# Performance work log

Hardware: AMD Instinct MI355X
Metric: run time of the kernel (lower is better)

## Reference

```python
import jax, jax.numpy as jnp
import numpy as np
import math

B, N, D, H = 4, 2048, 256, 4
DH = D // H
EPS = 1e-8


def setup_inputs() -> dict:
    key = jax.random.key(0)
    ks = jax.random.split(key, 8)
    x = jax.random.normal(ks[0], (B, N, D), dtype=jnp.float32)
    # RoPE rotation freqs: exp(i * pos * inv_freq), stored as (cos, sin) pairs -> [N, DH//2, 2]
    d2 = DH // 2
    inv_freq = 1.0 / (10000.0 ** (jnp.arange(d2, dtype=jnp.float32) / d2))
    ang = jnp.arange(N, dtype=jnp.float32)[:, None] * inv_freq[None, :]
    freqs = jnp.stack([jnp.cos(ang), jnp.sin(ang)], axis=-1)  # [N, d2, 2]
    s = 0.02
    g = jnp.ones((D,), dtype=jnp.float32)
    w_qkv = jax.random.normal(ks[1], (D, 3 * D), dtype=jnp.float32) * s
    b_qkv = jnp.zeros((3 * D,), dtype=jnp.float32)
    w_out = jax.random.normal(ks[2], (D, D), dtype=jnp.float32) * s
    b_out = jnp.zeros((D,), dtype=jnp.float32)
    w_gate = jax.random.normal(ks[3], (D, D), dtype=jnp.float32) * s
    b_gate = jnp.zeros((D,), dtype=jnp.float32)
    return {"x": x, "freqs": freqs, "g": g, "w_qkv": w_qkv, "b_qkv": b_qkv,
            "w_out": w_out, "b_out": b_out, "w_gate": w_gate, "b_gate": b_gate}


def _zcrmsnorm(x, g):
    x0 = x - jnp.mean(x, axis=-1, keepdims=True)
    rms = jnp.sqrt(jnp.mean(x0 * x0, axis=-1, keepdims=True) + EPS)
    return x0 / rms * g


def _rope(q, freqs):
    # q: [B,H,N,DH]; freqs: [N,DH//2,2] (cos,sin). Complex multiply on adjacent pairs.
    b, h, n, dh = q.shape
    qp = q.reshape(b, h, n, dh // 2, 2)
    cos = freqs[:n, :, 0][None, None]  # [1,1,N,d2]
    sin = freqs[:n, :, 1][None, None]
    q0, q1 = qp[..., 0], qp[..., 1]
    out = jnp.stack([q0 * cos - q1 * sin, q0 * sin + q1 * cos], axis=-1)
    return out.reshape(b, h, n, dh)


def reference(x, freqs, g, w_qkv, b_qkv, w_out, b_out, w_gate, b_gate):
    b, n, d = x.shape
    h = _zcrmsnorm(x, g)
    qkv = (h @ w_qkv + b_qkv).reshape(b, n, 3, H, DH)
    qkv = jnp.transpose(qkv, (2, 0, 3, 1, 4))  # [3,B,H,N,DH]
    q, k, v = qkv[0], qkv[1], qkv[2]
    q = _rope(q, freqs)
    k = _rope(k, freqs)
    scores = jnp.einsum('bhqd,bhkd->bhqk', q, k) / math.sqrt(DH)
    attn = jax.nn.softmax(scores, axis=-1)  # dropout is identity in eval
    y = jnp.einsum('bhqk,bhkd->bhqd', attn, v)
    y = jnp.transpose(y, (0, 2, 1, 3)).reshape(b, n, d)
    y = y @ w_out + b_out
    gate = jax.nn.sigmoid(h @ w_gate + b_gate)
    return x + gate * y
```

## Files before the change

### kernel.cpp

```cpp
#include <hip/hip_runtime.h>

typedef unsigned short u16;
typedef unsigned int u32;
typedef short short8 __attribute__((ext_vector_type(8)));
typedef float f32x4 __attribute__((ext_vector_type(4)));

#define B_ 4
#define N_ 2048
#define D_ 256
#define H_ 4
#define DH_ 64
#define BN_ 8192

__device__ inline float b2f(u16 u) {
    union { u32 i; float f; } v; v.i = ((u32)u) << 16; return v.f;
}
__device__ inline u16 f2b(float f) {
    union { float f; u32 i; } v; v.f = f;
    return (u16)((v.i + 0x8000u) >> 16);
}
__device__ inline u32 pkbf(float a, float b) {
    union { float f; u32 i; } ua, ub; ua.f = a; ub.f = b;
    return __builtin_amdgcn_perm(ub.i + 0x8000u, ua.i + 0x8000u, 0x07060302u);
}
__device__ inline f32x4 mfma16(short8 a, short8 b, f32x4 c) {
    return __builtin_amdgcn_mfma_f32_16x16x32_bf16(a, b, c, 0, 0, 0);
}

__device__ __forceinline__ void gemm_body(
    int bx, int by, int tid,
    const u16* __restrict__ A, const u16* __restrict__ BT,
    const float* __restrict__ bias, void* __restrict__ Cout,
    int Ntot)
{
    const int wave = tid >> 6, lane = tid & 63;
    const int ln15 = lane & 15, quad = lane >> 4;
    const int m0 = bx * 128 + (wave & 1) * 64;
    const int n0 = by * 128 + (wave >> 1) * 64;

    const f32x4 zero = {0.f, 0.f, 0.f, 0.f};
    f32x4 acc[4][4];
    #pragma unroll
    for (int i = 0; i < 4; ++i)
        #pragma unroll
        for (int j = 0; j < 4; ++j) acc[i][j] = zero;

    #pragma unroll
    for (int k0 = 0; k0 < 256; k0 += 32) {
        const int koff = k0 + quad * 8;
        short8 a[4], b[4];
        #pragma unroll
        for (int i = 0; i < 4; ++i)
            a[i] = *(const short8*)(A + (size_t)(m0 + i * 16 + ln15) * 256 + koff);
        #pragma unroll
        for (int j = 0; j < 4; ++j)
            b[j] = *(const short8*)(BT + (size_t)(n0 + j * 16 + ln15) * 256 + koff);
        #pragma unroll
        for (int i = 0; i < 4; ++i)
            #pragma unroll
            for (int j = 0; j < 4; ++j)
                acc[i][j] = mfma16(a[i], b[j], acc[i][j]);
    }

    #pragma unroll
    for (int i = 0; i < 4; ++i) {
        const int r = m0 + i * 16 + quad * 4;
        #pragma unroll
        for (int j = 0; j < 4; ++j) {
            const int c = n0 + j * 16 + ln15;
            const float bv = bias[c];
            #pragma unroll
            for (int rg = 0; rg < 4; ++rg) {
                const size_t idx = (size_t)(r + rg) * Ntot + c;
                ((u16*)Cout)[idx] = f2b(acc[i][j][rg] + bv);
            }
        }
    }
}

__device__ __forceinline__ void gemm_thin_body(
    int bx, int by, int tid,
    const u16* __restrict__ A, const u16* __restrict__ BT,
    const float* __restrict__ bias, void* __restrict__ Cout,
    const float* __restrict__ xin, const u16* __restrict__ gate,
    int mode)
{
    const int wave = tid >> 6, lane = tid & 63;
    const int ln15 = lane & 15, quad = lane >> 4;
    const int m0 = bx * 64 + (wave & 1) * 32;
    const int n0 = by * 64 + (wave >> 1) * 32;

    const f32x4 zero = {0.f, 0.f, 0.f, 0.f};
    f32x4 acc[2][2];
    #pragma unroll
    for (int i = 0; i < 2; ++i)
        #pragma unroll
        for (int j = 0; j < 2; ++j) acc[i][j] = zero;

    #pragma unroll
    for (int k0 = 0; k0 < 256; k0 += 32) {
        const int koff = k0 + quad * 8;
        short8 a[2], b[2];
        #pragma unroll
        for (int i = 0; i < 2; ++i)
            a[i] = *(const short8*)(A + (size_t)(m0 + i * 16 + ln15) * 256 + koff);
        #pragma unroll
        for (int j = 0; j < 2; ++j)
            b[j] = *(const short8*)(BT + (size_t)(n0 + j * 16 + ln15) * 256 + koff);
        #pragma unroll
        for (int i = 0; i < 2; ++i)
            #pragma unroll
            for (int j = 0; j < 2; ++j)
                acc[i][j] = mfma16(a[i], b[j], acc[i][j]);
    }

    #pragma unroll
    for (int i = 0; i < 2; ++i) {
        const int r = m0 + i * 16 + quad * 4;
        #pragma unroll
        for (int j = 0; j < 2; ++j) {
            const int c = n0 + j * 16 + ln15;
            const float bv = bias[c];
            #pragma unroll
            for (int rg = 0; rg < 4; ++rg) {
                const size_t idx = (size_t)(r + rg) * 256 + c;
                float v = acc[i][j][rg] + bv;
                if (mode == 1) {
                    ((u16*)Cout)[idx] = f2b(1.0f / (1.0f + __expf(-v)));
                } else {
                    ((float*)Cout)[idx] = xin[idx] + b2f(gate[idx]) * v;
                }
            }
        }
    }
}

__global__ __launch_bounds__(256) void gemm_ep(
    const u16* __restrict__ A, const u16* __restrict__ BT,
    const float* __restrict__ bias, void* __restrict__ Cout, int Ntot)
{
    gemm_body(blockIdx.x, blockIdx.y, threadIdx.x, A, BT, bias, Cout, Ntot);
}

__global__ __launch_bounds__(256) void gemm_thin(
    const u16* __restrict__ A, const u16* __restrict__ BT,
    const float* __restrict__ bias, void* __restrict__ Cout,
    const float* __restrict__ xin, const u16* __restrict__ gate, int mode)
{
    gemm_thin_body(blockIdx.x, blockIdx.y, threadIdx.x, A, BT, bias, Cout,
                   xin, gate, mode);
}

__global__ __launch_bounds__(256) void norm_transw_k(
    const float* __restrict__ x, const float* __restrict__ g, u16* __restrict__ h,
    const float* __restrict__ wqkv, const float* __restrict__ wout,
    const float* __restrict__ wgate,
    u16* __restrict__ wqkvT, u16* __restrict__ woutT, u16* __restrict__ wgateT)
{
    if (blockIdx.x < 2048) {
        const int wave = threadIdx.x >> 6, lane = threadIdx.x & 63;
        const int t = blockIdx.x * 4 + wave;
        const float4 u = *(const float4*)(x + (size_t)t * D_ + lane * 4);
        float s  = u.x + u.y + u.z + u.w;
        float s2 = u.x * u.x + u.y * u.y + u.z * u.z + u.w * u.w;
        #pragma unroll
        for (int m = 1; m < 64; m <<= 1) {
            s  += __shfl_xor(s, m);
            s2 += __shfl_xor(s2, m);
        }
        float mean = s * (1.0f / D_);
        float var  = s2 * (1.0f / D_) - mean * mean;
        float rinv = rsqrtf(var + 1e-8f);
        const float4 gv = *(const float4*)(g + lane * 4);
        uint2 o;
        o.x = pkbf((u.x - mean) * rinv * gv.x, (u.y - mean) * rinv * gv.y);
        o.y = pkbf((u.z - mean) * rinv * gv.z, (u.w - mean) * rinv * gv.w);
        *(uint2*)(h + (size_t)t * D_ + lane * 4) = o;
    } else {
        int idx = (blockIdx.x - 2048) * 256 + threadIdx.x;
        if (idx < 768 * 256) {
            int nn = idx >> 8, kk = idx & 255;
            wqkvT[idx] = f2b(wqkv[kk * 768 + nn]);
        }
        idx -= 768 * 256;
        if (idx >= 0 && idx < 256 * 256) {
            int nn = idx >> 8, kk = idx & 255;
            woutT[idx]  = f2b(wout[kk * 256 + nn]);
            wgateT[idx] = f2b(wgate[kk * 256 + nn]);
        }
    }
}

#define QSCALE 0.18033688f
__global__ __launch_bounds__(256) void rope_vt_gate_k(
    const u16* __restrict__ qkv, const float* __restrict__ freqs,
    u16* __restrict__ Q, u16* __restrict__ K, u16* __restrict__ VT,
    const u16* __restrict__ h, const u16* __restrict__ wgateT,
    const float* __restrict__ b_gate, u16* __restrict__ gatb)
{
    __shared__ __align__(16) u16 tile[64 * 65];
    const int blk = blockIdx.x;
    if (blk < 1024) {
        const int idx = blk * 256 + threadIdx.x;
        const int t = idx >> 5, rem = idx & 31;
        const int hh = rem >> 3, s8 = rem & 7;
        const int b = t >> 11, n = t & 2047;

        const float4 f0 = *(const float4*)(freqs + (size_t)n * 64 + s8 * 8);
        const float4 f1 = *(const float4*)(freqs + (size_t)n * 64 + s8 * 8 + 4);

        const u16* qp = qkv + (size_t)t * 768 + hh * 64 + s8 * 8;
        const uint4 qv = *(const uint4*)qp;
        const uint4 kv = *(const uint4*)(qp + 256);

        const size_t off = ((size_t)(b * H_ + hh) * N_ + n) * DH_ + s8 * 8;
        uint4 qo, ko;
        {
            float q0 = b2f((u16)(qv.x & 0xffff)), q1 = b2f((u16)(qv.x >> 16));
            float k0 = b2f((u16)(kv.x & 0xffff)), k1 = b2f((u16)(kv.x >> 16));
            qo.x = pkbf((q0 * f0.x - q1 * f0.y) * QSCALE, (q0 * f0.y + q1 * f0.x) * QSCALE);
            ko.x = pkbf(k0 * f0.x - k1 * f0.y, k0 * f0.y + k1 * f0.x);
        }
        {
            float q0 = b2f((u16)(qv.y & 0xffff)), q1 = b2f((u16)(qv.y >> 16));
            float k0 = b2f((u16)(kv.y & 0xffff)), k1 = b2f((u16)(kv.y >> 16));
            qo.y = pkbf((q0 * f0.z - q1 * f0.w) * QSCALE, (q0 * f0.w + q1 * f0.z) * QSCALE);
            ko.y = pkbf(k0 * f0.z - k1 * f0.w, k0 * f0.w + k1 * f0.z);
        }
        {
            float q0 = b2f((u16)(qv.z & 0xffff)), q1 = b2f((u16)(qv.z >> 16));
            float k0 = b2f((u16)(kv.z & 0xffff)), k1 = b2f((u16)(kv.z >> 16));
            qo.z = pkbf((q0 * f1.x - q1 * f1.y) * QSCALE, (q0 * f1.y + q1 * f1.x) * QSCALE);
            ko.z = pkbf(k0 * f1.x - k1 * f1.y, k0 * f1.y + k1 * f1.x);
        }
        {
            float q0 = b2f((u16)(qv.w & 0xffff)), q1 = b2f((u16)(qv.w >> 16));
            float k0 = b2f((u16)(kv.w & 0xffff)), k1 = b2f((u16)(kv.w >> 16));
            qo.w = pkbf((q0 * f1.z - q1 * f1.w) * QSCALE, (q0 * f1.w + q1 * f1.z) * QSCALE);
            ko.w = pkbf(k0 * f1.z - k1 * f1.w, k0 * f1.w + k1 * f1.z);
        }
        *(uint4*)(Q + off) = qo;
        *(uint4*)(K + off) = ko;
    } else if (blk < 1536) {
        const int id2 = blk - 1024;
        const int bh = id2 & 15;
        const int n0 = (id2 >> 4) * 64;
        const int b = bh >> 2, hh = bh & 3;
        #pragma unroll
        for (int rep = 0; rep < 16; ++rep) {
            int idx = rep * 256 + threadIdx.x;
            int nl = idx >> 6, dh = idx & 63;
            tile[dh * 65 + nl] = qkv[(size_t)(b * N_ + n0 + nl) * 768 + 512 + hh * 64 + dh];
        }
        __syncthreads();
        #pragma unroll
        for (int rep = 0; rep < 16; ++rep) {
            int idx = rep * 256 + threadIdx.x;
            int dh = idx >> 6, nl = idx & 63;
            VT[((size_t)bh * 64 + dh) * N_ + n0 + nl] = tile[dh * 65 + nl];
        }
    } else {
        const int id3 = blk - 1536;
        gemm_thin_body(id3 & 127, id3 >> 7, threadIdx.x, h, wgateT, b_gate,
                       (void*)gatb, (const float*)nullptr, (const u16*)nullptr, 1);
    }
}

__global__ __launch_bounds__(256) void attn_k(
    const u16* __restrict__ Q, const u16* __restrict__ K,
    const u16* __restrict__ VT, u16* __restrict__ yt)
{
    __shared__ __align__(16) u16 Ks[2][64][72];
    __shared__ __align__(16) u16 Vs[2][64][72];
    __shared__ __align__(16) u16 Pb[4][16 * 88];
    const int tid = threadIdx.x;
    const int wave = tid >> 6, lane = tid & 63;
    const int ln15 = lane & 15, quad = lane >> 4;
    const int id = blockIdx.x;
    const int bh = ((id & 7) << 1) | ((id >> 3) & 1);
    const int q0 = (id >> 4) * 64 + wave * 16;

    const u16* Qh = Q + (size_t)bh * N_ * DH_;
    const u16* Kh = K + (size_t)bh * N_ * DH_;
    const u16* Vh = VT + (size_t)bh * DH_ * N_;

    const short8 bq0 = *(const short8*)(Qh + (size_t)(q0 + ln15) * DH_ + quad * 8);
    const short8 bq1 = *(const short8*)(Qh + (size_t)(q0 + ln15) * DH_ + 32 + quad * 8);

    const f32x4 zero = {0.f, 0.f, 0.f, 0.f};
    f32x4 o[4];
    #pragma unroll
    for (int j = 0; j < 4; ++j) o[j] = zero;
    float lv = 0.f;
    u16* Pw = Pb[wave];

    const int srow = tid >> 2, sq4 = tid & 3;

    {
        uint4 k0 = *(const uint4*)(Kh + (size_t)srow * DH_ + sq4 * 8);
        uint4 k1 = *(const uint4*)(Kh + (size_t)srow * DH_ + (sq4 + 4) * 8);
        uint4 v0 = *(const uint4*)(Vh + (size_t)srow * N_ + sq4 * 8);
        uint4 v1 = *(const uint4*)(Vh + (size_t)srow * N_ + (sq4 + 4) * 8);
        *(uint4*)&Ks[0][srow][sq4 * 8] = k0;
        *(uint4*)&Ks[0][srow][(sq4 + 4) * 8] = k1;
        *(uint4*)&Vs[0][srow][sq4 * 8] = v0;
        *(uint4*)&Vs[0][srow][(sq4 + 4) * 8] = v1;
    }
    __syncthreads();

    int p = 0;
    for (int c = 0; c < 32; ++c) {
        const int ktn = (c + 1) * 64;
        uint4 k0, k1, v0, v1;
        const bool more = (c + 1 < 32);
        if (more) {
            k0 = *(const uint4*)(Kh + (size_t)(ktn + srow) * DH_ + sq4 * 8);
            k1 = *(const uint4*)(Kh + (size_t)(ktn + srow) * DH_ + (sq4 + 4) * 8);
            v0 = *(const uint4*)(Vh + (size_t)srow * N_ + ktn + sq4 * 8);
            v1 = *(const uint4*)(Vh + (size_t)srow * N_ + ktn + (sq4 + 4) * 8);
        }

        f32x4 st[4];
        #pragma unroll
        for (int c4 = 0; c4 < 4; ++c4) {
            short8 ka0 = *(const short8*)&Ks[p][c4 * 16 + ln15][quad * 8];
            short8 ka1 = *(const short8*)&Ks[p][c4 * 16 + ln15][32 + quad * 8];
            st[c4] = mfma16(ka0, bq0, zero);
            st[c4] = mfma16(ka1, bq1, st[c4]);
        }
        f32x4 pr[4];
        float rs = 0.f;
        #pragma unroll
        for (int c4 = 0; c4 < 4; ++c4) {
            #pragma unroll
            for (int r = 0; r < 4; ++r) {
                pr[c4][r] = exp2f(st[c4][r]);
                rs += pr[c4][r];
            }
        }
        lv += rs;
        #pragma unroll
        for (int c4 = 0; c4 < 4; ++c4) {
            uint2 w;
            w.x = pkbf(pr[c4][0], pr[c4][1]);
            w.y = pkbf(pr[c4][2], pr[c4][3]);
            *(uint2*)(Pw + ln15 * 88 + c4 * 16 + quad * 4) = w;
        }
        asm volatile("s_waitcnt lgkmcnt(0)" ::: "memory");
        const short8 bp0 = *(const short8*)(Pw + ln15 * 88 + quad * 8);
        const short8 bp1 = *(const short8*)(Pw + ln15 * 88 + 32 + quad * 8);
        #pragma unroll
        for (int j = 0; j < 4; ++j) {
            short8 va0 = *(const short8*)&Vs[p][j * 16 + ln15][quad * 8];
            short8 va1 = *(const short8*)&Vs[p][j * 16 + ln15][32 + quad * 8];
            o[j] = mfma16(va0, bp0, o[j]);
            o[j] = mfma16(va1, bp1, o[j]);
        }

        if (more) {
            *(uint4*)&Ks[p ^ 1][srow][sq4 * 8] = k0;
            *(uint4*)&Ks[p ^ 1][srow][(sq4 + 4) * 8] = k1;
            *(uint4*)&Vs[p ^ 1][srow][sq4 * 8] = v0;
            *(uint4*)&Vs[p ^ 1][srow][(sq4 + 4) * 8] = v1;
        }
        __syncthreads();
        p ^= 1;
    }

    lv += __shfl_xor(lv, 16);
    lv += __shfl_xor(lv, 32);
    const float rl = 1.0f / lv;
    const int b = bh >> 2, h = bh & 3;
    const size_t base = ((size_t)b * N_ + q0 + ln15) * D_ + h * 64;
    #pragma unroll
    for (int j = 0; j < 4; ++j) {
        uint2 w;
        w.x = pkbf(o[j][0] * rl, o[j][1] * rl);
        w.y = pkbf(o[j][2] * rl, o[j][3] * rl);
        *(uint2*)(yt + base + j * 16 + quad * 4) = w;
    }
}

extern "C" void kernel_launch(void* const* d_in, const int* in_sizes, int n_in,
                              void* d_out, int out_size, void* d_ws, size_t ws_size,
                              hipStream_t stream) {
    const float* x      = (const float*)d_in[0];
    const float* freqs  = (const float*)d_in[1];
    const float* g      = (const float*)d_in[2];
    const float* w_qkv  = (const float*)d_in[3];
    const float* b_qkv  = (const float*)d_in[4];
    const float* w_out  = (const float*)d_in[5];
    const float* b_out  = (const float*)d_in[6];
    const float* w_gate = (const float*)d_in[7];
    const float* b_gate = (const float*)d_in[8];
    float* out = (float*)d_out;

    char* ws = (char*)d_ws;
    size_t off = 0;
    auto carve = [&](size_t nelem) -> u16* {
        u16* p = (u16*)(ws + off);
        off += ((nelem * 2 + 255) / 256) * 256;
        return p;
    };
    u16* h      = carve((size_t)BN_ * D_);
    u16* qkv    = carve((size_t)BN_ * 768);
    u16* Qb     = carve((size_t)BN_ * D_);
    u16* Kb     = carve((size_t)BN_ * D_);
    u16* VT     = carve((size_t)BN_ * D_);
    u16* gatb   = carve((size_t)BN_ * D_);
    u16* wqkvT  = carve((size_t)768 * 256);
    u16* woutT  = carve((size_t)256 * 256);
    u16* wgateT = carve((size_t)256 * 256);
    u16* yt = qkv;

    hipLaunchKernelGGL(norm_transw_k, dim3(3072), dim3(256), 0, stream,
                       x, g, h, w_qkv, w_out, w_gate, wqkvT, woutT, wgateT);
    hipLaunchKernelGGL(gemm_ep, dim3(BN_ / 128, 6), dim3(256), 0, stream,
                       h, wqkvT, b_qkv, (void*)qkv, 768);
    hipLaunchKernelGGL(rope_vt_gate_k, dim3(2048), dim3(256), 0, stream,
                       qkv, freqs, Qb, Kb, VT, h, wgateT, b_gate, gatb);
    hipLaunchKernelGGL(attn_k, dim3(512), dim3(256), 0, stream,
                       Qb, Kb, VT, yt);
    hipLaunchKernelGGL(gemm_thin, dim3(128, 4), dim3(256), 0, stream,
                       yt, woutT, b_out, (void*)out, x, gatb, 2);
}
```

Before: 168.9 us.

## Split attention over key halves with 64-row query tiles per wave, merge in out-proj

Each attention wave now processes 64 query rows instead of 16, reusing every K/V tile loaded into shared memory across four query sub-tiles. The key range is split in two (split-K), giving 256 blocks that each cover half the keys. Unnormalised fp32 partial outputs and row sums go to workspace. The output-projection GEMM sums the two partials, normalises, and converts to bf16 while loading its A operand. This cuts shared-memory K/V traffic per query but adds register pressure, fewer blocks, and extra fp32 partial-output traffic through global memory.

```diff
diff --git a/kernel.cpp b/kernel.cpp
--- a/kernel.cpp
+++ b/kernel.cpp
@@ -81,9 +81,7 @@
 __device__ __forceinline__ void gemm_thin_body(
     int bx, int by, int tid,
     const u16* __restrict__ A, const u16* __restrict__ BT,
-    const float* __restrict__ bias, void* __restrict__ Cout,
-    const float* __restrict__ xin, const u16* __restrict__ gate,
-    int mode)
+    const float* __restrict__ bias, u16* __restrict__ Cout)
 {
     const int wave = tid >> 6, lane = tid & 63;
     const int ln15 = lane & 15, quad = lane >> 4;
@@ -123,13 +121,8 @@
             const float bv = bias[c];
             #pragma unroll
             for (int rg = 0; rg < 4; ++rg) {
-                const size_t idx = (size_t)(r + rg) * 256 + c;
                 float v = acc[i][j][rg] + bv;
-                if (mode == 1) {
-                    ((u16*)Cout)[idx] = f2b(1.0f / (1.0f + __expf(-v)));
-                } else {
-                    ((float*)Cout)[idx] = xin[idx] + b2f(gate[idx]) * v;
-                }
+                Cout[(size_t)(r + rg) * 256 + c] = f2b(1.0f / (1.0f + __expf(-v)));
             }
         }
     }
@@ -142,13 +135,72 @@
     gemm_body(blockIdx.x, blockIdx.y, threadIdx.x, A, BT, bias, Cout, Ntot);
 }
 
-__global__ __launch_bounds__(256) void gemm_thin(
-    const u16* __restrict__ A, const u16* __restrict__ BT,
-    const float* __restrict__ bias, void* __restrict__ Cout,
-    const float* __restrict__ xin, const u16* __restrict__ gate, int mode)
-{
-    gemm_thin_body(blockIdx.x, blockIdx.y, threadIdx.x, A, BT, bias, Cout,
-                   xin, gate, mode);
+__global__ __launch_bounds__(256) void out_gemm_k(
+    const float* __restrict__ o0, const float* __restrict__ o1,
+    const float* __restrict__ lv0, const float* __restrict__ lv1,
+    const u16* __restrict__ BT, const float* __restrict__ bias,
+    float* __restrict__ Cout, const float* __restrict__ xin,
+    const u16* __restrict__ gate)
+{
+    const int tid = threadIdx.x;
+    const int wave = tid >> 6, lane = tid & 63;
+    const int ln15 = lane & 15, quad = lane >> 4;
+    const int m0 = blockIdx.x * 64 + (wave & 1) * 32;
+    const int n0 = blockIdx.y * 64 + (wave >> 1) * 32;
+
+    const f32x4 zero = {0.f, 0.f, 0.f, 0.f};
+    f32x4 acc[2][2];
+    #pragma unroll
+    for (int i = 0; i < 2; ++i)
+        #pragma unroll
+        for (int j = 0; j < 2; ++j) acc[i][j] = zero;
+
+    #pragma unroll
+    for (int k0 = 0; k0 < 256; k0 += 32) {
+        const int koff = k0 + quad * 8;
+        const int head = k0 >> 6;
+        short8 a[2], b[2];
+        #pragma unroll
+        for (int i = 0; i < 2; ++i) {
+            const int m = m0 + i * 16 + ln15;
+            const float* p0 = o0 + (size_t)m * 256 + koff;
+            const float* p1 = o1 + (size_t)m * 256 + koff;
+            float4 a0 = *(const float4*)p0, a1 = *(const float4*)(p0 + 4);
+            float4 c0 = *(const float4*)p1, c1 = *(const float4*)(p1 + 4);
+            const int il = ((m >> 11) * 4 + head) * 2048 + (m & 2047);
+            const float rl = 1.0f / (lv0[il] + lv1[il]);
+            union { u32 u[4]; short8 s; } r;
+            r.u[0] = pkbf((a0.x + c0.x) * rl, (a0.y + c0.y) * rl);
+            r.u[1] = pkbf((a0.z + c0.z) * rl, (a0.w + c0.w) * rl);
+            r.u[2] = pkbf((a1.x + c1.x) * rl, (a1.y + c1.y) * rl);
+            r.u[3] = pkbf((a1.z + c1.z) * rl, (a1.w + c1.w) * rl);
+            a[i] = r.s;
+        }
+        #pragma unroll
+        for (int j = 0; j < 2; ++j)
+            b[j] = *(const short8*)(BT + (size_t)(n0 + j * 16 + ln15) * 256 + koff);
+        #pragma unroll
+        for (int i = 0; i < 2; ++i)
+            #pragma unroll
+            for (int j = 0; j < 2; ++j)
+                acc[i][j] = mfma16(a[i], b[j], acc[i][j]);
+    }
+
+    #pragma unroll
+    for (int i = 0; i < 2; ++i) {
+        const int r = m0 + i * 16 + quad * 4;
+        #pragma unroll
+        for (int j = 0; j < 2; ++j) {
+            const int c = n0 + j * 16 + ln15;
+            const float bv = bias[c];
+            #pragma unroll
+            for (int rg = 0; rg < 4; ++rg) {
+                const size_t idx = (size_t)(r + rg) * 256 + c;
+                float v = acc[i][j][rg] + bv;
+                Cout[idx] = xin[idx] + b2f(gate[idx]) * v;
+            }
+        }
+    }
 }
 
 __global__ __launch_bounds__(256) void norm_transw_k(
@@ -261,46 +313,56 @@
         }
     } else {
         const int id3 = blk - 1536;
-        gemm_thin_body(id3 & 127, id3 >> 7, threadIdx.x, h, wgateT, b_gate,
-                       (void*)gatb, (const float*)nullptr, (const u16*)nullptr, 1);
-    }
-}
-
-__global__ __launch_bounds__(256) void attn_k(
+        gemm_thin_body(id3 & 127, id3 >> 7, threadIdx.x, h, wgateT, b_gate, gatb);
+    }
+}
+
+__global__ __launch_bounds__(256, 1) void attn_k(
     const u16* __restrict__ Q, const u16* __restrict__ K,
-    const u16* __restrict__ VT, u16* __restrict__ yt)
+    const u16* __restrict__ VT, float* __restrict__ opart,
+    float* __restrict__ lvp)
 {
     __shared__ __align__(16) u16 Ks[2][64][72];
     __shared__ __align__(16) u16 Vs[2][64][72];
-    __shared__ __align__(16) u16 Pb[4][16 * 88];
+    __shared__ __align__(16) u16 Pb[4][64 * 72];
     const int tid = threadIdx.x;
     const int wave = tid >> 6, lane = tid & 63;
     const int ln15 = lane & 15, quad = lane >> 4;
     const int id = blockIdx.x;
     const int bh = ((id & 7) << 1) | ((id >> 3) & 1);
-    const int q0 = (id >> 4) * 64 + wave * 16;
+    const int rest = id >> 4;
+    const int qb = rest & 7, ks = rest >> 3;
+    const int q0w = qb * 256 + wave * 64;
 
     const u16* Qh = Q + (size_t)bh * N_ * DH_;
     const u16* Kh = K + (size_t)bh * N_ * DH_;
     const u16* Vh = VT + (size_t)bh * DH_ * N_;
 
-    const short8 bq0 = *(const short8*)(Qh + (size_t)(q0 + ln15) * DH_ + quad * 8);
-    const short8 bq1 = *(const short8*)(Qh + (size_t)(q0 + ln15) * DH_ + 32 + quad * 8);
+    short8 bq[4][2];
+    #pragma unroll
+    for (int qs = 0; qs < 4; ++qs) {
+        const u16* qp = Qh + (size_t)(q0w + qs * 16 + ln15) * DH_;
+        bq[qs][0] = *(const short8*)(qp + quad * 8);
+        bq[qs][1] = *(const short8*)(qp + 32 + quad * 8);
+    }
 
     const f32x4 zero = {0.f, 0.f, 0.f, 0.f};
-    f32x4 o[4];
-    #pragma unroll
-    for (int j = 0; j < 4; ++j) o[j] = zero;
-    float lv = 0.f;
+    f32x4 o[4][4];
+    #pragma unroll
+    for (int j = 0; j < 4; ++j)
+        #pragma unroll
+        for (int qs = 0; qs < 4; ++qs) o[j][qs] = zero;
+    float lv[4] = {0.f, 0.f, 0.f, 0.f};
     u16* Pw = Pb[wave];
 
+    const int kbeg = ks * (N_ / 2);
     const int srow = tid >> 2, sq4 = tid & 3;
 
     {
-        uint4 k0 = *(const uint4*)(Kh + (size_t)srow * DH_ + sq4 * 8);
-        uint4 k1 = *(const uint4*)(Kh + (size_t)srow * DH_ + (sq4 + 4) * 8);
-        uint4 v0 = *(const uint4*)(Vh + (size_t)srow * N_ + sq4 * 8);
-        uint4 v1 = *(const uint4*)(Vh + (size_t)srow * N_ + (sq4 + 4) * 8);
+        uint4 k0 = *(const uint4*)(Kh + (size_t)(kbeg + srow) * DH_ + sq4 * 8);
+        uint4 k1 = *(const uint4*)(Kh + (size_t)(kbeg + srow) * DH_ + (sq4 + 4) * 8);
+        uint4 v0 = *(const uint4*)(Vh + (size_t)srow * N_ + kbeg + sq4 * 8);
+        uint4 v1 = *(const uint4*)(Vh + (size_t)srow * N_ + kbeg + (sq4 + 4) * 8);
         *(uint4*)&Ks[0][srow][sq4 * 8] = k0;
         *(uint4*)&Ks[0][srow][(sq4 + 4) * 8] = k1;
         *(uint4*)&Vs[0][srow][sq4 * 8] = v0;
@@ -309,10 +371,10 @@
     __syncthreads();
 
     int p = 0;
-    for (int c = 0; c < 32; ++c) {
-        const int ktn = (c + 1) * 64;
+    for (int c = 0; c < 16; ++c) {
+        const int ktn = kbeg + (c + 1) * 64;
         uint4 k0, k1, v0, v1;
-        const bool more = (c + 1 < 32);
+        const bool more = (c + 1 < 16);
         if (more) {
             k0 = *(const uint4*)(Kh + (size_t)(ktn + srow) * DH_ + sq4 * 8);
             k1 = *(const uint4*)(Kh + (size_t)(ktn + srow) * DH_ + (sq4 + 4) * 8);
@@ -320,41 +382,50 @@
             v1 = *(const uint4*)(Vh + (size_t)srow * N_ + ktn + (sq4 + 4) * 8);
         }
 
-        f32x4 st[4];
+        short8 ka[4][2];
         #pragma unroll
         for (int c4 = 0; c4 < 4; ++c4) {
-            short8 ka0 = *(const short8*)&Ks[p][c4 * 16 + ln15][quad * 8];
-            short8 ka1 = *(const short8*)&Ks[p][c4 * 16 + ln15][32 + quad * 8];
-            st[c4] = mfma16(ka0, bq0, zero);
-            st[c4] = mfma16(ka1, bq1, st[c4]);
-        }
-        f32x4 pr[4];
-        float rs = 0.f;
-        #pragma unroll
-        for (int c4 = 0; c4 < 4; ++c4) {
-            #pragma unroll
-            for (int r = 0; r < 4; ++r) {
-                pr[c4][r] = exp2f(st[c4][r]);
-                rs += pr[c4][r];
+            ka[c4][0] = *(const short8*)&Ks[p][c4 * 16 + ln15][quad * 8];
+            ka[c4][1] = *(const short8*)&Ks[p][c4 * 16 + ln15][32 + quad * 8];
+        }
+        #pragma unroll
+        for (int qs = 0; qs < 4; ++qs) {
+            f32x4 st[4];
+            #pragma unroll
+            for (int c4 = 0; c4 < 4; ++c4) {
+                st[c4] = mfma16(ka[c4][0], bq[qs][0], zero);
+                st[c4] = mfma16(ka[c4][1], bq[qs][1], st[c4]);
             }
-        }
-        lv += rs;
-        #pragma unroll
-        for (int c4 = 0; c4 < 4; ++c4) {
-            uint2 w;
-            w.x = pkbf(pr[c4][0], pr[c4][1]);
-            w.y = pkbf(pr[c4][2], pr[c4][3]);
-            *(uint2*)(Pw + ln15 * 88 + c4 * 16 + quad * 4) = w;
+            float rs = 0.f;
+            #pragma unroll
+            for (int c4 = 0; c4 < 4; ++c4) {
+                f32x4 pr;
+                #pragma unroll
+                for (int r = 0; r < 4; ++r) { pr[r] = exp2f(st[c4][r]); rs += pr[r]; }
+                uint2 w;
+                w.x = pkbf(pr[0], pr[1]);
+                w.y = pkbf(pr[2], pr[3]);
+                *(uint2*)(Pw + (qs * 16 + ln15) * 72 + c4 * 16 + quad * 4) = w;
+            }
+            lv[qs] += rs;
         }
         asm volatile("s_waitcnt lgkmcnt(0)" ::: "memory");
-        const short8 bp0 = *(const short8*)(Pw + ln15 * 88 + quad * 8);
-        const short8 bp1 = *(const short8*)(Pw + ln15 * 88 + 32 + quad * 8);
+
+        short8 va[4][2];
         #pragma unroll
         for (int j = 0; j < 4; ++j) {
-            short8 va0 = *(const short8*)&Vs[p][j * 16 + ln15][quad * 8];
-            short8 va1 = *(const short8*)&Vs[p][j * 16 + ln15][32 + quad * 8];
-            o[j] = mfma16(va0, bp0, o[j]);
-            o[j] = mfma16(va1, bp1, o[j]);
+            va[j][0] = *(const short8*)&Vs[p][j * 16 + ln15][quad * 8];
+            va[j][1] = *(const short8*)&Vs[p][j * 16 + ln15][32 + quad * 8];
+        }
+        #pragma unroll
+        for (int qs = 0; qs < 4; ++qs) {
+            const short8 bp0 = *(const short8*)(Pw + (qs * 16 + ln15) * 72 + quad * 8);
+            const short8 bp1 = *(const short8*)(Pw + (qs * 16 + ln15) * 72 + 32 + quad * 8);
+            #pragma unroll
+            for (int j = 0; j < 4; ++j) {
+                o[j][qs] = mfma16(va[j][0], bp0, o[j][qs]);
+                o[j][qs] = mfma16(va[j][1], bp1, o[j][qs]);
+            }
         }
 
         if (more) {
@@ -367,17 +438,28 @@
         p ^= 1;
     }
 
-    lv += __shfl_xor(lv, 16);
-    lv += __shfl_xor(lv, 32);
-    const float rl = 1.0f / lv;
+    #pragma unroll
+    for (int qs = 0; qs < 4; ++qs) {
+        lv[qs] += __shfl_xor(lv[qs], 16);
+        lv[qs] += __shfl_xor(lv[qs], 32);
+    }
     const int b = bh >> 2, h = bh & 3;
-    const size_t base = ((size_t)b * N_ + q0 + ln15) * D_ + h * 64;
-    #pragma unroll
-    for (int j = 0; j < 4; ++j) {
-        uint2 w;
-        w.x = pkbf(o[j][0] * rl, o[j][1] * rl);
-        w.y = pkbf(o[j][2] * rl, o[j][3] * rl);
-        *(uint2*)(yt + base + j * 16 + quad * 4) = w;
+    if (quad == 0) {
+        #pragma unroll
+        for (int qs = 0; qs < 4; ++qs)
+            lvp[(size_t)ks * 32768 + bh * 2048 + q0w + qs * 16 + ln15] = lv[qs];
+    }
+    float* op = opart + (size_t)ks * BN_ * D_;
+    #pragma unroll
+    for (int qs = 0; qs < 4; ++qs) {
+        const size_t tok = (size_t)b * N_ + q0w + qs * 16 + ln15;
+        #pragma unroll
+        for (int j = 0; j < 4; ++j) {
+            float4 w;
+            w.x = o[j][qs][0]; w.y = o[j][qs][1];
+            w.z = o[j][qs][2]; w.w = o[j][qs][3];
+            *(float4*)(op + tok * D_ + h * 64 + j * 16 + quad * 4) = w;
+        }
     }
 }
 
@@ -397,21 +479,22 @@
 
     char* ws = (char*)d_ws;
     size_t off = 0;
-    auto carve = [&](size_t nelem) -> u16* {
-        u16* p = (u16*)(ws + off);
-        off += ((nelem * 2 + 255) / 256) * 256;
+    auto carveB = [&](size_t bytes) -> char* {
+        char* p = ws + off;
+        off += (bytes + 255) & ~(size_t)255;
         return p;
     };
-    u16* h      = carve((size_t)BN_ * D_);
-    u16* qkv    = carve((size_t)BN_ * 768);
-    u16* Qb     = carve((size_t)BN_ * D_);
-    u16* Kb     = carve((size_t)BN_ * D_);
-    u16* VT     = carve((size_t)BN_ * D_);
-    u16* gatb   = carve((size_t)BN_ * D_);
-    u16* wqkvT  = carve((size_t)768 * 256);
-    u16* woutT  = carve((size_t)256 * 256);
-    u16* wgateT = carve((size_t)256 * 256);
-    u16* yt = qkv;
+    u16* h      = (u16*)carveB((size_t)BN_ * D_ * 2);
+    u16* qkv    = (u16*)carveB((size_t)BN_ * 768 * 2);
+    u16* Qb     = (u16*)carveB((size_t)BN_ * D_ * 2);
+    u16* Kb     = (u16*)carveB((size_t)BN_ * D_ * 2);
+    u16* VT     = (u16*)carveB((size_t)BN_ * D_ * 2);
+    u16* gatb   = (u16*)carveB((size_t)BN_ * D_ * 2);
+    u16* wqkvT  = (u16*)carveB((size_t)768 * 256 * 2);
+    u16* woutT  = (u16*)carveB((size_t)256 * 256 * 2);
+    u16* wgateT = (u16*)carveB((size_t)256 * 256 * 2);
+    float* opart = (float*)carveB((size_t)2 * BN_ * D_ * 4);
+    float* lvp   = (float*)carveB((size_t)2 * 16 * N_ * 4);
 
     hipLaunchKernelGGL(norm_transw_k, dim3(3072), dim3(256), 0, stream,
                        x, g, h, w_qkv, w_out, w_gate, wqkvT, woutT, wgateT);
@@ -419,8 +502,9 @@
                        h, wqkvT, b_qkv, (void*)qkv, 768);
     hipLaunchKernelGGL(rope_vt_gate_k, dim3(2048), dim3(256), 0, stream,
                        qkv, freqs, Qb, Kb, VT, h, wgateT, b_gate, gatb);
-    hipLaunchKernelGGL(attn_k, dim3(512), dim3(256), 0, stream,
-                       Qb, Kb, VT, yt);
-    hipLaunchKernelGGL(gemm_thin, dim3(128, 4), dim3(256), 0, stream,
-                       yt, woutT, b_out, (void*)out, x, gatb, 2);
-}
+    hipLaunchKernelGGL(attn_k, dim3(256), dim3(256), 0, stream,
+                       Qb, Kb, VT, opart, lvp);
+    hipLaunchKernelGGL(out_gemm_k, dim3(BN_ / 64, 4), dim3(256), 0, stream,
+                       opart, opart + (size_t)BN_ * D_, lvp, lvp + 32768,
+                       woutT, b_out, out, x, gatb);
+}
```

Result: slower. 179.0 us (+6.0%).
